# Kernel optimization log

Measured on AMD Instinct MI355X. Metric: run time of the kernel, lower is better.

Reference implementation:

```python
import jax, jax.numpy as jnp
import numpy as np

DIM = 1024
HEADS = 16
DIM_HEAD = 64
SCALE = DIM_HEAD ** -0.5
RMS_SCALE = DIM ** 0.5


def rms_norm(x, gamma):
    # F.normalize(x, dim=-1) * sqrt(dim) * gamma
    norm = jnp.sqrt(jnp.sum(x * x, axis=-1, keepdims=True))
    normed = x / jnp.maximum(norm, 1e-12)
    return normed * RMS_SCALE * gamma


def setup_inputs() -> dict:
    key = jax.random.key(0)
    ks = jax.random.split(key, 7)
    b, n, m = 2, 2048, 2048
    x = jax.random.normal(ks[0], (b, n, DIM), dtype=jnp.float32)
    context = jax.random.normal(ks[1], (b, m, DIM), dtype=jnp.float32)
    normalized_scores_kv = jax.random.uniform(ks[2], (b, m), dtype=jnp.float32)
    mask = jnp.ones((b, m), dtype=bool)
    gamma = jnp.ones((DIM,), dtype=jnp.float32)
    s = 0.02
    Wq = jax.random.normal(ks[3], (DIM, HEADS * DIM_HEAD), dtype=jnp.float32) * s
    Wkv = jax.random.normal(ks[4], (DIM, 2 * HEADS * DIM_HEAD), dtype=jnp.float32) * s
    Wout = jax.random.normal(ks[5], (HEADS * DIM_HEAD, DIM), dtype=jnp.float32) * s
    return {"x": x, "context": context, "normalized_scores_kv": normalized_scores_kv,
            "mask": mask, "gamma": gamma, "Wq": Wq, "Wkv": Wkv, "Wout": Wout}


def reference(x, context, normalized_scores_kv, mask, gamma, Wq, Wkv, Wout):
    b, n, _ = x.shape
    m = context.shape[1]
    xn = rms_norm(x, gamma)
    cn = rms_norm(context, gamma)
    q = xn @ Wq                     # [b, n, h*d]
    kv = cn @ Wkv                   # [b, m, 2*h*d]
    k, v = jnp.split(kv, 2, axis=-1)
    def to_heads(t):
        return t.reshape(t.shape[0], t.shape[1], HEADS, DIM_HEAD).transpose(0, 2, 1, 3)
    q, k, v = to_heads(q), to_heads(k), to_heads(v)   # [b, h, n, d]
    v = v * normalized_scores_kv[:, None, :, None]
    q = q * SCALE
    sim = jnp.einsum('bhid,bhjd->bhij', q, k)
    neg = -jnp.finfo(sim.dtype).max
    sim = jnp.where(mask[:, None, None, :], sim, neg)
    attn = jax.nn.softmax(sim, axis=-1)
    out = jnp.einsum('bhij,bhjd->bhid', attn, v)
    out = out.transpose(0, 2, 1, 3).reshape(b, n, HEADS * DIM_HEAD)
    return out @ Wout
```

## Files before the change

kernel.cpp:

```cpp
#include <hip/hip_runtime.h>
#include <hip/hip_bf16.h>

typedef _Float16 f16;
typedef _Float16 f16x4 __attribute__((ext_vector_type(4)));
typedef _Float16 f16x8 __attribute__((ext_vector_type(8)));
typedef float f32x4 __attribute__((ext_vector_type(4)));

#define DIM 1024
#define SEQ 2048
#define NB 2
#define NH 16
#define DHEAD 64
#define KVB 64
#define QBLK 256

__global__ __launch_bounds__(256) void rms_cast_kernel(
    const float* __restrict__ x, const float* __restrict__ ctx,
    const float* __restrict__ gamma, f16* __restrict__ xn, f16* __restrict__ cn)
{
  int row = blockIdx.x;
  const float* src; f16* dst;
  if (row < NB * SEQ) { src = x + (size_t)row * DIM;              dst = xn + (size_t)row * DIM; }
  else                { src = ctx + (size_t)(row - NB*SEQ) * DIM; dst = cn + (size_t)(row - NB*SEQ) * DIM; }
  int t = threadIdx.x;
  float4 v = ((const float4*)src)[t];
  float ss = v.x*v.x + v.y*v.y + v.z*v.z + v.w*v.w;
  #pragma unroll
  for (int m = 1; m < 64; m <<= 1) ss += __shfl_xor(ss, m, 64);
  __shared__ float red[4];
  if ((t & 63) == 0) red[t >> 6] = ss;
  __syncthreads();
  float total = red[0] + red[1] + red[2] + red[3];
  float scale = 32.0f / fmaxf(sqrtf(total), 1e-12f);
  float4 gv = ((const float4*)gamma)[t];
  dst[4*t+0] = (f16)(v.x * scale * gv.x);
  dst[4*t+1] = (f16)(v.y * scale * gv.y);
  dst[4*t+2] = (f16)(v.z * scale * gv.z);
  dst[4*t+3] = (f16)(v.w * scale * gv.w);
}

__global__ __launch_bounds__(256) void transpose_cast3_kernel(
    const float* __restrict__ Wq, const float* __restrict__ Wkv, const float* __restrict__ Wout,
    f16* __restrict__ WqT, f16* __restrict__ WkvT, f16* __restrict__ WoT)
{
  __shared__ float tile[32][33];
  int bx = blockIdx.x;
  const float* W; f16* Wt; int N, n0;
  if (bx < 32)      { W = Wq;   Wt = WqT;  N = 1024; n0 = bx * 32; }
  else if (bx < 96) { W = Wkv;  Wt = WkvT; N = 2048; n0 = (bx - 32) * 32; }
  else              { W = Wout; Wt = WoT;  N = 1024; n0 = (bx - 96) * 32; }
  int k0 = blockIdx.y * 32;
  int tx = threadIdx.x & 31, ty = threadIdx.x >> 5;
  #pragma unroll
  for (int i = 0; i < 32; i += 8)
    tile[ty + i][tx] = W[(size_t)(k0 + ty + i) * N + n0 + tx];
  __syncthreads();
  #pragma unroll
  for (int i = 0; i < 32; i += 8)
    Wt[(size_t)(n0 + ty + i) * 1024 + k0 + tx] = (f16)tile[tx][ty + i];
}

template<int MODE>
__global__ __launch_bounds__(256) void gemm_kernel(
    const f16* __restrict__ A, const f16* __restrict__ Bt,
    const float* __restrict__ scores,
    f16* __restrict__ o16a, f16* __restrict__ o16b, float* __restrict__ o32)
{
  __shared__ f16 As[128][40];
  __shared__ f16 Bs[128][40];
  const int m0 = blockIdx.x * 128, n0 = blockIdx.y * 128;
  const int tid = threadIdx.x, lane = tid & 63, w = tid >> 6;
  const int wm = w >> 1, wn = w & 1;
  const int g = lane >> 4, c = lane & 15;
  const int srow = tid >> 1, skc = (tid & 1) * 16;

  const f16* pa = A  + (size_t)(m0 + srow) * 1024 + skc;
  const f16* pb = Bt + (size_t)(n0 + srow) * 1024 + skc;

  f32x4 acc[4][4] = {};

  float4 ra0 = ((const float4*)pa)[0], ra1 = ((const float4*)pa)[1];
  float4 rb0 = ((const float4*)pb)[0], rb1 = ((const float4*)pb)[1];

  for (int k0 = 0; k0 < 1024; k0 += 32) {
    __syncthreads();
    *(float4*)&As[srow][skc]     = ra0;
    *(float4*)&As[srow][skc + 8] = ra1;
    *(float4*)&Bs[srow][skc]     = rb0;
    *(float4*)&Bs[srow][skc + 8] = rb1;
    if (k0 + 32 < 1024) {
      const f16* qa = pa + k0 + 32; const f16* qb = pb + k0 + 32;
      ra0 = ((const float4*)qa)[0]; ra1 = ((const float4*)qa)[1];
      rb0 = ((const float4*)qb)[0]; rb1 = ((const float4*)qb)[1];
    }
    __syncthreads();
    f16x8 af[4], bf[4];
    #pragma unroll
    for (int tm = 0; tm < 4; tm++) af[tm] = *(const f16x8*)&As[wm*64 + tm*16 + c][g*8];
    #pragma unroll
    for (int tn = 0; tn < 4; tn++) bf[tn] = *(const f16x8*)&Bs[wn*64 + tn*16 + c][g*8];
    #pragma unroll
    for (int tm = 0; tm < 4; tm++)
      #pragma unroll
      for (int tn = 0; tn < 4; tn++)
        acc[tm][tn] = __builtin_amdgcn_mfma_f32_16x16x32_f16(af[tm], bf[tn], acc[tm][tn], 0, 0, 0);
  }

  #pragma unroll
  for (int tm = 0; tm < 4; tm++) {
    #pragma unroll
    for (int tn = 0; tn < 4; tn++) {
      int rg0 = m0 + wm*64 + tm*16 + g*4;
      int cg  = n0 + wn*64 + tn*16 + c;
      int b = rg0 >> 11, s0 = rg0 & 2047;
      if (MODE == 0) {
        int h = cg >> 6, d = cg & 63;
        #pragma unroll
        for (int r = 0; r < 4; r++)
          o16a[(((size_t)(b*NH + h))*SEQ + s0 + r)*DHEAD + d] =
              (f16)(acc[tm][tn][r] * 0.18033688011112043f);
      } else if (MODE == 1) {
        int hh = (cg & 1023) >> 6, d = cg & 63;
        if (cg < 1024) {
          #pragma unroll
          for (int r = 0; r < 4; r++)
            o16a[(((size_t)(b*NH + hh))*SEQ + s0 + r)*DHEAD + d] = (f16)acc[tm][tn][r];
        } else {
          float4 sc = *(const float4*)(scores + b*SEQ + s0);
          f16x4 pk;
          pk[0] = (f16)(acc[tm][tn][0] * sc.x);
          pk[1] = (f16)(acc[tm][tn][1] * sc.y);
          pk[2] = (f16)(acc[tm][tn][2] * sc.z);
          pk[3] = (f16)(acc[tm][tn][3] * sc.w);
          *(f16x4*)(o16b + (((size_t)(b*NH + hh))*DHEAD + d)*SEQ + s0) = pk;
        }
      } else {
        #pragma unroll
        for (int r = 0; r < 4; r++)
          o32[(size_t)(rg0 + r) * 1024 + cg] = acc[tm][tn][r];
      }
    }
  }
}

#define KS_OFF 0
#define VT_OFF 8192
#define PT_OFF 17408

__global__ __launch_bounds__(512, 2) void attn_kernel(
    const f16* __restrict__ Q, const f16* __restrict__ K,
    const f16* __restrict__ Vt, f16* __restrict__ O)
{
  __shared__ __align__(16) char L[54272];

  const int bid = blockIdx.x;
  const int bh   = ((bid & 7) << 2) | ((bid >> 3) & 3);
  const int q0   = (bid >> 5) * QBLK;
  const int tid = threadIdx.x, lane = tid & 63, w = tid >> 6;
  const int g = lane >> 4, c = lane & 15;

  const f16* Qb  = Q  + (size_t)bh * SEQ * DHEAD;
  const f16* Kb  = K  + (size_t)bh * SEQ * DHEAD;
  const f16* Vbt = Vt + (size_t)bh * DHEAD * SEQ;

  f16x8 aq[2][2];
  #pragma unroll
  for (int qs = 0; qs < 2; qs++) {
    int qr = q0 + w*32 + qs*16 + c;
    aq[qs][0] = *(const f16x8*)(Qb + (size_t)qr * DHEAD + g*8);
    aq[qs][1] = *(const f16x8*)(Qb + (size_t)qr * DHEAD + 32 + g*8);
  }

  f32x4 oacc[2][4] = {};
  float mr[2] = {-1e30f, -1e30f};
  float lr[2] = {0.f, 0.f};

  const int strow = tid >> 3, stch = tid & 7;
  const f16* kg = Kb  + (size_t)strow * DHEAD + stch * 8;
  const f16* vg = Vbt + (size_t)strow * SEQ   + stch * 8;
  const unsigned kswz = KS_OFF + strow*128 + ((stch ^ (strow & 7)) << 4);
  const unsigned vswz = VT_OFF + strow*144 + stch*16;
  const unsigned ptb  = PT_OFF + w*4608;

  float4 kr = *(const float4*)kg;
  float4 vr = *(const float4*)vg;

  for (int kv0 = 0; kv0 < SEQ; kv0 += KVB) {
    __syncthreads();
    *(float4*)(L + kswz) = kr;
    *(float4*)(L + vswz) = vr;
    __syncthreads();

    if (kv0 + KVB < SEQ) {
      kr = *(const float4*)(kg + (size_t)(kv0 + KVB) * DHEAD);
      vr = *(const float4*)(vg + kv0 + KVB);
    }

    f32x4 s[4][2] = {};
    __builtin_amdgcn_s_setprio(1);
    #pragma unroll
    for (int ct = 0; ct < 4; ct++) {
      #pragma unroll
      for (int kc = 0; kc < 2; kc++) {
        f16x8 kf = *(const f16x8*)(L + KS_OFF + (ct*16 + c)*128 + (((kc*4 + g) ^ (c & 7)) << 4));
        s[ct][0] = __builtin_amdgcn_mfma_f32_16x16x32_f16(kf, aq[0][kc], s[ct][0], 0, 0, 0);
        s[ct][1] = __builtin_amdgcn_mfma_f32_16x16x32_f16(kf, aq[1][kc], s[ct][1], 0, 0, 0);
      }
    }
    __builtin_amdgcn_s_setprio(0);

    #pragma unroll
    for (int qs = 0; qs < 2; qs++) {
      float mx = -1e30f;
      #pragma unroll
      for (int ct = 0; ct < 4; ct++)
        mx = fmaxf(mx, fmaxf(fmaxf(s[ct][qs][0], s[ct][qs][1]), fmaxf(s[ct][qs][2], s[ct][qs][3])));
      mx = fmaxf(mx, __shfl_xor(mx, 16, 64));
      mx = fmaxf(mx, __shfl_xor(mx, 32, 64));
      float mn = fmaxf(mr[qs], mx);
      float al = __builtin_amdgcn_exp2f(mr[qs] - mn);
      mr[qs] = mn;
      float rs = 0.f;
      #pragma unroll
      for (int ct = 0; ct < 4; ct++) {
        #pragma unroll
        for (int r = 0; r < 4; r++) {
          float p = __builtin_amdgcn_exp2f(s[ct][qs][r] - mn);
          s[ct][qs][r] = p; rs += p;
        }
      }
      rs += __shfl_xor(rs, 16, 64);
      rs += __shfl_xor(rs, 32, 64);
      lr[qs] = lr[qs] * al + rs;
      #pragma unroll
      for (int dt = 0; dt < 4; dt++)
        #pragma unroll
        for (int r = 0; r < 4; r++) oacc[qs][dt][r] *= al;

      #pragma unroll
      for (int ct = 0; ct < 4; ct++) {
        f16x4 pk;
        pk[0] = (f16)s[ct][qs][0]; pk[1] = (f16)s[ct][qs][1];
        pk[2] = (f16)s[ct][qs][2]; pk[3] = (f16)s[ct][qs][3];
        *(f16x4*)(L + ptb + (qs*16 + c)*144 + ct*32 + g*8) = pk;
      }
    }

    __builtin_amdgcn_s_setprio(1);
    #pragma unroll
    for (int kc = 0; kc < 2; kc++) {
      f16x8 bp0 = *(const f16x8*)(L + ptb + c*144        + kc*64 + g*16);
      f16x8 bp1 = *(const f16x8*)(L + ptb + (16 + c)*144 + kc*64 + g*16);
      #pragma unroll
      for (int dt = 0; dt < 4; dt++) {
        f16x8 vf = *(const f16x8*)(L + VT_OFF + (dt*16 + c)*144 + kc*64 + g*16);
        oacc[0][dt] = __builtin_amdgcn_mfma_f32_16x16x32_f16(vf, bp0, oacc[0][dt], 0, 0, 0);
        oacc[1][dt] = __builtin_amdgcn_mfma_f32_16x16x32_f16(vf, bp1, oacc[1][dt], 0, 0, 0);
      }
    }
    __builtin_amdgcn_s_setprio(0);
  }

  #pragma unroll
  for (int qs = 0; qs < 2; qs++) {
    float inv = 1.0f / lr[qs];
    #pragma unroll
    for (int dt = 0; dt < 4; dt++) {
      f16x4 pk;
      pk[0] = (f16)(oacc[qs][dt][0] * inv);
      pk[1] = (f16)(oacc[qs][dt][1] * inv);
      pk[2] = (f16)(oacc[qs][dt][2] * inv);
      pk[3] = (f16)(oacc[qs][dt][3] * inv);
      *(f16x4*)(L + ptb + (qs*16 + c)*144 + (dt*16 + 4*g)*2) = pk;
    }
  }
  {
    const int b = bh >> 4, h = bh & 15;
    #pragma unroll
    for (int p = 0; p < 2; p++) {
      int ql = p*16 + (lane >> 2), chq = lane & 3;
      const char* src = L + ptb + ql*144 + chq*32;
      float4 a0 = *(const float4*)src;
      float4 a1 = *(const float4*)(src + 16);
      f16* dst = O + ((size_t)(b*SEQ + q0 + w*32 + ql))*1024 + h*64 + chq*16;
      *(float4*)dst = a0;
      *(float4*)(dst + 8) = a1;
    }
  }
}

extern "C" void kernel_launch(void* const* d_in, const int* in_sizes, int n_in,
                              void* d_out, int out_size, void* d_ws, size_t ws_size,
                              hipStream_t stream)
{
  const float* x      = (const float*)d_in[0];
  const float* ctx    = (const float*)d_in[1];
  const float* scores = (const float*)d_in[2];
  const float* gamma  = (const float*)d_in[4];
  const float* Wq     = (const float*)d_in[5];
  const float* Wkv    = (const float*)d_in[6];
  const float* Wout   = (const float*)d_in[7];
  float* out = (float*)d_out;

  char* ws = (char*)d_ws;
  const size_t MB = 1024 * 1024;
  f16* xn   = (f16*)(ws);
  f16* cn   = (f16*)(ws + 8*MB);
  f16* WqT  = (f16*)(ws + 16*MB);
  f16* WkvT = (f16*)(ws + 18*MB);
  f16* WoT  = (f16*)(ws + 22*MB);
  f16* qb   = (f16*)(ws + 24*MB);
  f16* kb   = (f16*)(ws + 32*MB);
  f16* vbT  = (f16*)(ws + 40*MB);
  f16* ao   = xn;

  rms_cast_kernel<<<NB*SEQ*2, 256, 0, stream>>>(x, ctx, gamma, xn, cn);
  transpose_cast3_kernel<<<dim3(128, 32), 256, 0, stream>>>(Wq, Wkv, Wout, WqT, WkvT, WoT);
  gemm_kernel<0><<<dim3(32, 8),  256, 0, stream>>>(xn, WqT,  nullptr, qb, nullptr, nullptr);
  gemm_kernel<1><<<dim3(32, 16), 256, 0, stream>>>(cn, WkvT, scores,  kb, vbT,     nullptr);
  attn_kernel<<<dim3(256), 512, 0, stream>>>(qb, kb, vbT, ao);
  gemm_kernel<2><<<dim3(32, 8),  256, 0, stream>>>(ao, WoT,  nullptr, nullptr, nullptr, out);
}
```

Before: 147.5 us.

## Split attention KV across waves and pipeline GEMM with direct global-to-LDS loads

The attention kernel now gives each 256-thread block 64 query rows. Each of the four waves handles a disjoint quarter of the KV sequence, reading K and V fragments straight from global memory into registers. The per-wave softmax states are merged through LDS at the end, and online rescaling is skipped when the running max grows by at most 8. The GEMM switches to double-buffered global_load_lds staging with 64-wide K steps, a swizzled LDS layout and two blocks per CU. These changes are meant to remove block-wide barriers and LDS staging of K/V, raise the number of blocks, and overlap loads with MFMA work. The cost is a cross-wave reduction epilogue, larger LDS use, and uncoalesced per-lane global fragment loads.

Measured after the change: 140.9 us. 4.5% less time.

```diff
diff --git a/kernel.cpp b/kernel.cpp
--- a/kernel.cpp
+++ b/kernel.cpp
@@ -2,8 +2,10 @@
 #include <hip/hip_bf16.h>
 
 typedef _Float16 f16;
+typedef _Float16 f16x2 __attribute__((ext_vector_type(2)));
 typedef _Float16 f16x4 __attribute__((ext_vector_type(4)));
 typedef _Float16 f16x8 __attribute__((ext_vector_type(8)));
+typedef __fp16 h16x2 __attribute__((ext_vector_type(2)));
 typedef float f32x4 __attribute__((ext_vector_type(4)));
 
 #define DIM 1024
@@ -11,8 +13,17 @@
 #define NB 2
 #define NH 16
 #define DHEAD 64
-#define KVB 64
-#define QBLK 256
+
+__device__ __forceinline__ void gl_lds16(const f16* g, f16* l) {
+  __builtin_amdgcn_global_load_lds(
+      (const __attribute__((address_space(1))) unsigned int*)(g),
+      (__attribute__((address_space(3))) unsigned int*)(l), 16, 0, 0);
+}
+
+__device__ __forceinline__ f16x2 pkrtz(float a, float b) {
+  h16x2 t = __builtin_amdgcn_cvt_pkrtz(a, b);
+  return __builtin_bit_cast(f16x2, t);
+}
 
 __global__ __launch_bounds__(256) void rms_cast_kernel(
     const float* __restrict__ x, const float* __restrict__ ctx,
@@ -61,50 +72,60 @@
 }
 
 template<int MODE>
-__global__ __launch_bounds__(256) void gemm_kernel(
+__global__ __launch_bounds__(256, 2) void gemm_kernel(
     const f16* __restrict__ A, const f16* __restrict__ Bt,
     const float* __restrict__ scores,
     f16* __restrict__ o16a, f16* __restrict__ o16b, float* __restrict__ o32)
 {
-  __shared__ f16 As[128][40];
-  __shared__ f16 Bs[128][40];
+  __shared__ __align__(16) char L[65536];
+
   const int m0 = blockIdx.x * 128, n0 = blockIdx.y * 128;
   const int tid = threadIdx.x, lane = tid & 63, w = tid >> 6;
   const int wm = w >> 1, wn = w & 1;
   const int g = lane >> 4, c = lane & 15;
-  const int srow = tid >> 1, skc = (tid & 1) * 16;
-
-  const f16* pa = A  + (size_t)(m0 + srow) * 1024 + skc;
-  const f16* pb = Bt + (size_t)(n0 + srow) * 1024 + skc;
+
+  const int sj = lane >> 3;
+  const int sl = (lane & 7) ^ sj;
+  const f16* gA = A  + (size_t)(m0 + w*32 + sj) * 1024 + sl * 8;
+  const f16* gB = Bt + (size_t)(n0 + w*32 + sj) * 1024 + sl * 8;
+  const unsigned stA = w * 4096;
+  const unsigned stB = 16384 + w * 4096;
+
+  const unsigned swz = (c & 7) << 4;
 
   f32x4 acc[4][4] = {};
 
-  float4 ra0 = ((const float4*)pa)[0], ra1 = ((const float4*)pa)[1];
-  float4 rb0 = ((const float4*)pb)[0], rb1 = ((const float4*)pb)[1];
-
-  for (int k0 = 0; k0 < 1024; k0 += 32) {
+#define GSTAGE(k0v, buf) {                                                      \
+    _Pragma("unroll")                                                           \
+    for (int i2 = 0; i2 < 4; i2++) {                                            \
+      gl_lds16(gA + (size_t)(8*i2) * 1024 + (k0v), (f16*)(L + (buf) + stA + i2*1024)); \
+      gl_lds16(gB + (size_t)(8*i2) * 1024 + (k0v), (f16*)(L + (buf) + stB + i2*1024)); \
+    } }
+
+  GSTAGE(0, 0)
+  __syncthreads();
+
+  for (int t = 0; t < 16; ++t) {
+    const unsigned cur = (t & 1) ? 32768u : 0u;
+    if (t + 1 < 16) GSTAGE((t + 1) * 64, cur ^ 32768u)
+    #pragma unroll
+    for (int kk = 0; kk < 2; kk++) {
+      f16x8 af[4], bf[4];
+      #pragma unroll
+      for (int tm = 0; tm < 4; tm++)
+        af[tm] = *(const f16x8*)(L + cur + (wm*64 + tm*16 + c)*128 + (((kk*4 + g) << 4) ^ swz));
+      #pragma unroll
+      for (int tn = 0; tn < 4; tn++)
+        bf[tn] = *(const f16x8*)(L + cur + 16384 + (wn*64 + tn*16 + c)*128 + (((kk*4 + g) << 4) ^ swz));
+      #pragma unroll
+      for (int tm = 0; tm < 4; tm++)
+        #pragma unroll
+        for (int tn = 0; tn < 4; tn++)
+          acc[tm][tn] = __builtin_amdgcn_mfma_f32_16x16x32_f16(af[tm], bf[tn], acc[tm][tn], 0, 0, 0);
+    }
     __syncthreads();
-    *(float4*)&As[srow][skc]     = ra0;
-    *(float4*)&As[srow][skc + 8] = ra1;
-    *(float4*)&Bs[srow][skc]     = rb0;
-    *(float4*)&Bs[srow][skc + 8] = rb1;
-    if (k0 + 32 < 1024) {
-      const f16* qa = pa + k0 + 32; const f16* qb = pb + k0 + 32;
-      ra0 = ((const float4*)qa)[0]; ra1 = ((const float4*)qa)[1];
-      rb0 = ((const float4*)qb)[0]; rb1 = ((const float4*)qb)[1];
-    }
-    __syncthreads();
-    f16x8 af[4], bf[4];
-    #pragma unroll
-    for (int tm = 0; tm < 4; tm++) af[tm] = *(const f16x8*)&As[wm*64 + tm*16 + c][g*8];
-    #pragma unroll
-    for (int tn = 0; tn < 4; tn++) bf[tn] = *(const f16x8*)&Bs[wn*64 + tn*16 + c][g*8];
-    #pragma unroll
-    for (int tm = 0; tm < 4; tm++)
-      #pragma unroll
-      for (int tn = 0; tn < 4; tn++)
-        acc[tm][tn] = __builtin_amdgcn_mfma_f32_16x16x32_f16(af[tm], bf[tn], acc[tm][tn], 0, 0, 0);
-  }
+  }
+#undef GSTAGE
 
   #pragma unroll
   for (int tm = 0; tm < 4; tm++) {
@@ -143,19 +164,20 @@
   }
 }
 
-#define KS_OFF 0
-#define VT_OFF 8192
-#define PT_OFF 17408
-
-__global__ __launch_bounds__(512, 2) void attn_kernel(
+#define PT 0
+#define ML 20480
+#define MBUF 22528
+
+__global__ __launch_bounds__(256, 2) void attn_kernel(
     const f16* __restrict__ Q, const f16* __restrict__ K,
     const f16* __restrict__ Vt, f16* __restrict__ O)
 {
-  __shared__ __align__(16) char L[54272];
+  __shared__ __align__(16) char L[55296];
 
   const int bid = blockIdx.x;
-  const int bh   = ((bid & 7) << 2) | ((bid >> 3) & 3);
-  const int q0   = (bid >> 5) * QBLK;
+  const int xcd = bid & 7, ii = bid >> 3;
+  const int bh  = xcd*4 + (ii >> 5);
+  const int q0  = (ii & 31) * 64;
   const int tid = threadIdx.x, lane = tid & 63, w = tid >> 6;
   const int g = lane >> 4, c = lane & 15;
 
@@ -163,128 +185,169 @@
   const f16* Kb  = K  + (size_t)bh * SEQ * DHEAD;
   const f16* Vbt = Vt + (size_t)bh * DHEAD * SEQ;
 
-  f16x8 aq[2][2];
-  #pragma unroll
-  for (int qs = 0; qs < 2; qs++) {
-    int qr = q0 + w*32 + qs*16 + c;
-    aq[qs][0] = *(const f16x8*)(Qb + (size_t)qr * DHEAD + g*8);
-    aq[qs][1] = *(const f16x8*)(Qb + (size_t)qr * DHEAD + 32 + g*8);
-  }
-
-  f32x4 oacc[2][4] = {};
-  float mr[2] = {-1e30f, -1e30f};
-  float lr[2] = {0.f, 0.f};
-
-  const int strow = tid >> 3, stch = tid & 7;
-  const f16* kg = Kb  + (size_t)strow * DHEAD + stch * 8;
-  const f16* vg = Vbt + (size_t)strow * SEQ   + stch * 8;
-  const unsigned kswz = KS_OFF + strow*128 + ((stch ^ (strow & 7)) << 4);
-  const unsigned vswz = VT_OFF + strow*144 + stch*16;
-  const unsigned ptb  = PT_OFF + w*4608;
-
-  float4 kr = *(const float4*)kg;
-  float4 vr = *(const float4*)vg;
-
-  for (int kv0 = 0; kv0 < SEQ; kv0 += KVB) {
-    __syncthreads();
-    *(float4*)(L + kswz) = kr;
-    *(float4*)(L + vswz) = vr;
-    __syncthreads();
-
-    if (kv0 + KVB < SEQ) {
-      kr = *(const float4*)(kg + (size_t)(kv0 + KVB) * DHEAD);
-      vr = *(const float4*)(vg + kv0 + KVB);
-    }
-
-    f32x4 s[4][2] = {};
+  f16x8 bq[4][2];
+  #pragma unroll
+  for (int qs = 0; qs < 4; qs++)
+    #pragma unroll
+    for (int kc = 0; kc < 2; kc++)
+      bq[qs][kc] = *(const f16x8*)(Qb + (size_t)(q0 + qs*16 + c)*DHEAD + kc*32 + g*8);
+
+  const f16* kfp = Kb  + (size_t)(w*32 + c)*DHEAD + g*8;
+  const f16* vfp = Vbt + (size_t)c*SEQ + w*32 + g*8;
+
+  f32x4 oacc[4][4] = {};
+  float mr[4] = {-1e30f,-1e30f,-1e30f,-1e30f};
+  float lr[4] = {0.f, 0.f, 0.f, 0.f};
+
+  const unsigned ptb = PT + w*5120;
+
+  f16x8 kf[2][2], vf[4];
+  #pragma unroll
+  for (int ks = 0; ks < 2; ks++)
+    #pragma unroll
+    for (int kc = 0; kc < 2; kc++)
+      kf[ks][kc] = *(const f16x8*)(kfp + ks*16*DHEAD + kc*32);
+  #pragma unroll
+  for (int dt = 0; dt < 4; dt++)
+    vf[dt] = *(const f16x8*)(vfp + (size_t)dt*16*SEQ);
+
+  for (int t = 0; t < 16; ++t) {
+    f32x4 s[2][4];
     __builtin_amdgcn_s_setprio(1);
     #pragma unroll
-    for (int ct = 0; ct < 4; ct++) {
-      #pragma unroll
-      for (int kc = 0; kc < 2; kc++) {
-        f16x8 kf = *(const f16x8*)(L + KS_OFF + (ct*16 + c)*128 + (((kc*4 + g) ^ (c & 7)) << 4));
-        s[ct][0] = __builtin_amdgcn_mfma_f32_16x16x32_f16(kf, aq[0][kc], s[ct][0], 0, 0, 0);
-        s[ct][1] = __builtin_amdgcn_mfma_f32_16x16x32_f16(kf, aq[1][kc], s[ct][1], 0, 0, 0);
-      }
-    }
+    for (int ks = 0; ks < 2; ks++)
+      #pragma unroll
+      for (int qs = 0; qs < 4; qs++) {
+        f32x4 z = {0.f, 0.f, 0.f, 0.f};
+        z          = __builtin_amdgcn_mfma_f32_16x16x32_f16(kf[ks][0], bq[qs][0], z, 0, 0, 0);
+        s[ks][qs]  = __builtin_amdgcn_mfma_f32_16x16x32_f16(kf[ks][1], bq[qs][1], z, 0, 0, 0);
+      }
     __builtin_amdgcn_s_setprio(0);
-
-    #pragma unroll
-    for (int qs = 0; qs < 2; qs++) {
-      float mx = -1e30f;
-      #pragma unroll
-      for (int ct = 0; ct < 4; ct++)
-        mx = fmaxf(mx, fmaxf(fmaxf(s[ct][qs][0], s[ct][qs][1]), fmaxf(s[ct][qs][2], s[ct][qs][3])));
-      mx = fmaxf(mx, __shfl_xor(mx, 16, 64));
-      mx = fmaxf(mx, __shfl_xor(mx, 32, 64));
-      float mn = fmaxf(mr[qs], mx);
-      float al = __builtin_amdgcn_exp2f(mr[qs] - mn);
-      mr[qs] = mn;
+    if (t + 1 < 16) {
+      #pragma unroll
+      for (int ks = 0; ks < 2; ks++)
+        #pragma unroll
+        for (int kc = 0; kc < 2; kc++)
+          kf[ks][kc] = *(const f16x8*)(kfp + (size_t)(t+1)*128*DHEAD + ks*16*DHEAD + kc*32);
+    }
+
+    float mx[4];
+    #pragma unroll
+    for (int qs = 0; qs < 4; qs++) {
+      float m0v = fmaxf(fmaxf(s[0][qs][0], s[0][qs][1]), fmaxf(s[0][qs][2], s[0][qs][3]));
+      float m1v = fmaxf(fmaxf(s[1][qs][0], s[1][qs][1]), fmaxf(s[1][qs][2], s[1][qs][3]));
+      float m = fmaxf(m0v, m1v);
+      m = fmaxf(m, __shfl_xor(m, 16, 64));
+      m = fmaxf(m, __shfl_xor(m, 32, 64));
+      mx[qs] = m;
+    }
+    bool ok = (mx[0] <= mr[0] + 8.f) && (mx[1] <= mr[1] + 8.f) &&
+              (mx[2] <= mr[2] + 8.f) && (mx[3] <= mr[3] + 8.f);
+    if (!__all(ok)) {
+      #pragma unroll
+      for (int qs = 0; qs < 4; qs++) {
+        float mn = fmaxf(mr[qs], mx[qs]);
+        float al = __builtin_amdgcn_exp2f(mr[qs] - mn);
+        mr[qs] = mn; lr[qs] *= al;
+        #pragma unroll
+        for (int dt = 0; dt < 4; dt++) {
+          oacc[dt][qs][0] *= al; oacc[dt][qs][1] *= al;
+          oacc[dt][qs][2] *= al; oacc[dt][qs][3] *= al;
+        }
+      }
+    }
+    #pragma unroll
+    for (int qs = 0; qs < 4; qs++) {
       float rs = 0.f;
       #pragma unroll
-      for (int ct = 0; ct < 4; ct++) {
-        #pragma unroll
-        for (int r = 0; r < 4; r++) {
-          float p = __builtin_amdgcn_exp2f(s[ct][qs][r] - mn);
-          s[ct][qs][r] = p; rs += p;
-        }
+      for (int ks = 0; ks < 2; ks++) {
+        float p0 = __builtin_amdgcn_exp2f(s[ks][qs][0] - mr[qs]);
+        float p1 = __builtin_amdgcn_exp2f(s[ks][qs][1] - mr[qs]);
+        float p2 = __builtin_amdgcn_exp2f(s[ks][qs][2] - mr[qs]);
+        float p3 = __builtin_amdgcn_exp2f(s[ks][qs][3] - mr[qs]);
+        rs += (p0 + p1) + (p2 + p3);
+        f16x2 lo = pkrtz(p0, p1), hi = pkrtz(p2, p3);
+        f16x4 pk = __builtin_shufflevector(lo, hi, 0, 1, 2, 3);
+        *(f16x4*)(L + ptb + (qs*16 + c)*80 + ks*32 + g*8) = pk;
       }
       rs += __shfl_xor(rs, 16, 64);
       rs += __shfl_xor(rs, 32, 64);
-      lr[qs] = lr[qs] * al + rs;
+      lr[qs] += rs;
+    }
+
+    f16x8 bp[4];
+    #pragma unroll
+    for (int qs = 0; qs < 4; qs++)
+      bp[qs] = *(const f16x8*)(L + ptb + (qs*16 + c)*80 + g*16);
+    __builtin_amdgcn_s_setprio(1);
+    #pragma unroll
+    for (int dt = 0; dt < 4; dt++)
+      #pragma unroll
+      for (int qs = 0; qs < 4; qs++)
+        oacc[dt][qs] = __builtin_amdgcn_mfma_f32_16x16x32_f16(vf[dt], bp[qs], oacc[dt][qs], 0, 0, 0);
+    __builtin_amdgcn_s_setprio(0);
+    if (t + 1 < 16) {
       #pragma unroll
       for (int dt = 0; dt < 4; dt++)
-        #pragma unroll
-        for (int r = 0; r < 4; r++) oacc[qs][dt][r] *= al;
-
-      #pragma unroll
-      for (int ct = 0; ct < 4; ct++) {
-        f16x4 pk;
-        pk[0] = (f16)s[ct][qs][0]; pk[1] = (f16)s[ct][qs][1];
-        pk[2] = (f16)s[ct][qs][2]; pk[3] = (f16)s[ct][qs][3];
-        *(f16x4*)(L + ptb + (qs*16 + c)*144 + ct*32 + g*8) = pk;
-      }
-    }
-
-    __builtin_amdgcn_s_setprio(1);
-    #pragma unroll
-    for (int kc = 0; kc < 2; kc++) {
-      f16x8 bp0 = *(const f16x8*)(L + ptb + c*144        + kc*64 + g*16);
-      f16x8 bp1 = *(const f16x8*)(L + ptb + (16 + c)*144 + kc*64 + g*16);
-      #pragma unroll
-      for (int dt = 0; dt < 4; dt++) {
-        f16x8 vf = *(const f16x8*)(L + VT_OFF + (dt*16 + c)*144 + kc*64 + g*16);
-        oacc[0][dt] = __builtin_amdgcn_mfma_f32_16x16x32_f16(vf, bp0, oacc[0][dt], 0, 0, 0);
-        oacc[1][dt] = __builtin_amdgcn_mfma_f32_16x16x32_f16(vf, bp1, oacc[1][dt], 0, 0, 0);
-      }
-    }
-    __builtin_amdgcn_s_setprio(0);
-  }
-
-  #pragma unroll
-  for (int qs = 0; qs < 2; qs++) {
-    float inv = 1.0f / lr[qs];
-    #pragma unroll
-    for (int dt = 0; dt < 4; dt++) {
-      f16x4 pk;
-      pk[0] = (f16)(oacc[qs][dt][0] * inv);
-      pk[1] = (f16)(oacc[qs][dt][1] * inv);
-      pk[2] = (f16)(oacc[qs][dt][2] * inv);
-      pk[3] = (f16)(oacc[qs][dt][3] * inv);
-      *(f16x4*)(L + ptb + (qs*16 + c)*144 + (dt*16 + 4*g)*2) = pk;
-    }
-  }
-  {
-    const int b = bh >> 4, h = bh & 15;
-    #pragma unroll
-    for (int p = 0; p < 2; p++) {
-      int ql = p*16 + (lane >> 2), chq = lane & 3;
-      const char* src = L + ptb + ql*144 + chq*32;
-      float4 a0 = *(const float4*)src;
-      float4 a1 = *(const float4*)(src + 16);
-      f16* dst = O + ((size_t)(b*SEQ + q0 + w*32 + ql))*1024 + h*64 + chq*16;
-      *(float4*)dst = a0;
-      *(float4*)(dst + 8) = a1;
+        vf[dt] = *(const f16x8*)(vfp + (size_t)dt*16*SEQ + (t+1)*128);
+    }
+  }
+
+  if (g == 0) {
+    #pragma unroll
+    for (int qs = 0; qs < 4; qs++) {
+      *(float*)(L + ML + (w*2 + 0)*256 + (qs*16 + c)*4) = mr[qs];
+      *(float*)(L + ML + (w*2 + 1)*256 + (qs*16 + c)*4) = lr[qs];
+    }
+  }
+  __syncthreads();
+  float fw[4];
+  #pragma unroll
+  for (int qs = 0; qs < 4; qs++) {
+    float mwv[4], lwv[4];
+    #pragma unroll
+    for (int ww = 0; ww < 4; ww++) {
+      mwv[ww] = *(const float*)(L + ML + (ww*2 + 0)*256 + (qs*16 + c)*4);
+      lwv[ww] = *(const float*)(L + ML + (ww*2 + 1)*256 + (qs*16 + c)*4);
+    }
+    float M = fmaxf(fmaxf(mwv[0], mwv[1]), fmaxf(mwv[2], mwv[3]));
+    float Ls = lwv[0]*__builtin_amdgcn_exp2f(mwv[0]-M) + lwv[1]*__builtin_amdgcn_exp2f(mwv[1]-M)
+             + lwv[2]*__builtin_amdgcn_exp2f(mwv[2]-M) + lwv[3]*__builtin_amdgcn_exp2f(mwv[3]-M);
+    fw[qs] = __builtin_amdgcn_exp2f(mr[qs] - M) / Ls;
+  }
+
+  const int b = bh >> 4, h = bh & 15;
+  #pragma unroll
+  for (int pass = 0; pass < 2; ++pass) {
+    __syncthreads();
+    #pragma unroll
+    for (int dh = 0; dh < 2; dh++) {
+      int dt = pass*2 + dh;
+      #pragma unroll
+      for (int qs = 0; qs < 4; qs++) {
+        f32x4 v;
+        v[0] = oacc[dt][qs][0] * fw[qs]; v[1] = oacc[dt][qs][1] * fw[qs];
+        v[2] = oacc[dt][qs][2] * fw[qs]; v[3] = oacc[dt][qs][3] * fw[qs];
+        unsigned chunk = (unsigned)((dh*4 + g) ^ (c & 7));
+        *(f32x4*)(L + MBUF + w*8192 + (qs*16 + c)*128 + chunk*16) = v;
+      }
+    }
+    __syncthreads();
+    int q = tid >> 2, cp = tid & 3;
+    #pragma unroll
+    for (int j = 0; j < 2; j++) {
+      int ch = cp*2 + j;
+      unsigned pch = (unsigned)(ch ^ (q & 7));
+      f32x4 s0 = *(const f32x4*)(L + MBUF +         q*128 + pch*16);
+      f32x4 s1 = *(const f32x4*)(L + MBUF +  8192 + q*128 + pch*16);
+      f32x4 s2 = *(const f32x4*)(L + MBUF + 16384 + q*128 + pch*16);
+      f32x4 s3 = *(const f32x4*)(L + MBUF + 24576 + q*128 + pch*16);
+      f16x4 o;
+      o[0] = (f16)(s0[0]+s1[0]+s2[0]+s3[0]);
+      o[1] = (f16)(s0[1]+s1[1]+s2[1]+s3[1]);
+      o[2] = (f16)(s0[2]+s1[2]+s2[2]+s3[2]);
+      o[3] = (f16)(s0[3]+s1[3]+s2[3]+s3[3]);
+      *(f16x4*)(O + ((size_t)(b*SEQ + q0 + q))*1024 + h*64 + pass*32 + ch*4) = o;
     }
   }
 }
@@ -318,6 +381,6 @@
   transpose_cast3_kernel<<<dim3(128, 32), 256, 0, stream>>>(Wq, Wkv, Wout, WqT, WkvT, WoT);
   gemm_kernel<0><<<dim3(32, 8),  256, 0, stream>>>(xn, WqT,  nullptr, qb, nullptr, nullptr);
   gemm_kernel<1><<<dim3(32, 16), 256, 0, stream>>>(cn, WkvT, scores,  kb, vbT,     nullptr);
-  attn_kernel<<<dim3(256), 512, 0, stream>>>(qb, kb, vbT, ao);
+  attn_kernel<<<dim3(1024), 256, 0, stream>>>(qb, kb, vbT, ao);
   gemm_kernel<2><<<dim3(32, 8),  256, 0, stream>>>(ao, WoT,  nullptr, nullptr, nullptr, out);
 }
```
